# Kernel optimization log

Hardware: AMD Instinct MI355X
Metric: run time of the kernel (lower is better)

The kernel has to match this reference:

```python
import jax, jax.numpy as jnp
import numpy as np

N = 200_000   # num_nodes
E = 100_000   # events per direction
D = 128       # memory_dim
F = 128       # event feature dim
T = 128       # time encoding dim


def setup_inputs() -> dict:
    key = jax.random.key(0)
    ks = jax.random.split(key, 12)
    src = jax.random.randint(ks[0], (E,), 0, N)
    dst = jax.random.randint(ks[1], (E,), 0, N)
    t = jax.random.uniform(ks[2], (E,)) * 1000.0
    feat = jax.random.normal(ks[3], (E, F))
    memory = jax.random.normal(ks[4], (N, D)) * 0.1
    last_update = jnp.zeros((N,), dtype=jnp.float32)
    time_w = jax.random.normal(ks[5], (T,)) * 0.1
    time_b = jax.random.normal(ks[6], (T,)) * 0.1
    M = 2 * D + T + F  # message dim = 512
    w_ih = jax.random.normal(ks[7], (3 * D, M)) * 0.02
    w_hh = jax.random.normal(ks[8], (3 * D, D)) * 0.02
    b_ih = jnp.zeros((3 * D,), dtype=jnp.float32)
    b_hh = jnp.zeros((3 * D,), dtype=jnp.float32)
    return {
        "memory": memory, "last_update": last_update, "t": t, "feat": feat,
        "time_w": time_w, "time_b": time_b,
        "w_ih": w_ih, "w_hh": w_hh, "b_ih": b_ih, "b_hh": b_hh,
        "src": src, "dst": dst,
    }


def time_encode(dt, w, b):
    # TGN/TGAT-style cosine time encoding: [E] -> [E, T]
    return jnp.cos(dt[:, None] * w[None, :] + b[None, :])


def gru_cell(x, h, w_ih, w_hh, b_ih, b_hh):
    # Standard torch.nn.GRUCell math (gates ordered r, z, n).
    gi = x @ w_ih.T + b_ih  # [N, 3D]
    gh = h @ w_hh.T + b_hh  # [N, 3D]
    i_r, i_z, i_n = jnp.split(gi, 3, axis=-1)
    h_r, h_z, h_n = jnp.split(gh, 3, axis=-1)
    r = jax.nn.sigmoid(i_r + h_r)
    z = jax.nn.sigmoid(i_z + h_z)
    n = jnp.tanh(i_n + r * h_n)
    return (1.0 - z) * n + z * h


def reference(memory, last_update, t, feat, time_w, time_b,
              w_ih, w_hh, b_ih, b_hh, src, dst):
    # --- message functions (identity = concat), both directions ---
    s_msg = jnp.concatenate(
        [memory[src], memory[dst], time_encode(t - last_update[src], time_w, time_b), feat], axis=-1)
    d_msg = jnp.concatenate(
        [memory[dst], memory[src], time_encode(t - last_update[dst], time_w, time_b), feat], axis=-1)

    nodes = jnp.concatenate([src, dst], axis=0)        # [2E]
    te = jnp.concatenate([t, t], axis=0)               # [2E]
    msg = jnp.concatenate([s_msg, d_msg], axis=0)      # [2E, M]

    # --- 'last' aggregator: per-node argmax over event time (scatter_max) ---
    # Stable sort by time; segment_max over sorted positions yields, per node,
    # the latest event (ties broken toward the later original index).
    perm = jnp.argsort(te, stable=True)                # [2E]
    pos = jnp.arange(2 * E)
    best_pos = jax.ops.segment_max(pos, nodes[perm], num_segments=N)  # [N], intmin if empty
    has_msg = best_pos >= 0
    best = perm[jnp.clip(best_pos, 0)]                 # [N] event index of latest msg

    agg_msg = msg[best]                                # [N, M] gather
    max_t = te[best]                                   # [N]

    # --- GRU memory update + masked scatter back into memory ---
    new_mem = gru_cell(agg_msg, memory, w_ih, w_hh, b_ih, b_hh)
    new_memory = jnp.where(has_msg[:, None], new_mem, memory)
    new_last_update = jnp.where(has_msg, max_t, last_update)
    return new_memory, new_last_update
```

## Files before the change

### kernel.cpp

```cpp
#include <hip/hip_runtime.h>
#include <hip/hip_bf16.h>
#include <stdint.h>

typedef __hip_bfloat16 bf16;
typedef unsigned long long u64;
typedef unsigned int u32;
typedef short short8 __attribute__((ext_vector_type(8)));
typedef float f32x4 __attribute__((ext_vector_type(4)));

#define D_ 128
#define K_ 640
#define BM 64
#define BN 128
#define BK 64
#define BM2 32

__device__ __forceinline__ float bf2f(bf16 v) { return __bfloat162float(v); }
__device__ __forceinline__ u32 fbits(float f) { union { float f; u32 u; } c; c.f = f; return c.u; }
__device__ __forceinline__ u32 pk2(float a, float b) {
  union { bf16 h; unsigned short s; } x, y;
  x.h = __float2bfloat16(a); y.h = __float2bfloat16(b);
  return (u32)x.s | ((u32)y.s << 16);
}
template<bool F32>
__device__ __forceinline__ float ldE(const void* p, size_t i) {
  return F32 ? ((const float*)p)[i] : bf2f(((const bf16*)p)[i]);
}
template<bool F32>
__device__ __forceinline__ void stE(void* p, size_t i, float v) {
  if (F32) ((float*)p)[i] = v; else ((bf16*)p)[i] = __float2bfloat16(v);
}
template<bool F32>
__device__ __forceinline__ uint4 ld8(const void* base, size_t elemOff) {
  if (!F32) {
    return *(const uint4*)((const bf16*)base + elemOff);
  } else {
    const float4* p = (const float4*)((const float*)base + elemOff);
    float4 v0 = p[0], v1 = p[1];
    uint4 o; o.x = pk2(v0.x, v0.y); o.y = pk2(v0.z, v0.w);
    o.z = pk2(v1.x, v1.y); o.w = pk2(v1.z, v1.w);
    return o;
  }
}
template<bool F32>
__device__ __forceinline__ void stage8(const void* base, size_t elemOff, bf16* dst) {
  *(uint4*)dst = ld8<F32>(base, elemOff);
}
__device__ __forceinline__ void gl_lds16(const void* g, void* l) {
  __builtin_amdgcn_global_load_lds(
      (const __attribute__((address_space(1))) unsigned int*)g,
      (__attribute__((address_space(3))) unsigned int*)l, 16, 0, 0);
}

__global__ void k_prep(u64* __restrict__ key, u32* __restrict__ cnt, int N,
                       const u32* __restrict__ mem_w, const u32* __restrict__ t_w,
                       u32* __restrict__ flag) {
  int i = blockIdx.x * blockDim.x + threadIdx.x;
  if (i < N) key[i] = 0ull;
  if (i == 0) {
    *cnt = 0u;
    int ok = 1;
    for (int k = 0; k < 64; ++k) {
      u32 w = mem_w[k];
      if ((w & 0x7fffu) > 0x4300u) ok = 0;
      if (((w >> 16) & 0x7fffu) > 0x4300u) ok = 0;
    }
    for (int k = 0; k < 16; ++k) {
      u32 w = t_w[k];
      if ((w & 0xffffu) > 0x4480u) ok = 0;
      if ((w >> 16) > 0x4480u) ok = 0;
    }
    *flag = ok ? 0u : 1u;
  }
}

__global__ void k_scat(const int* __restrict__ src, const int* __restrict__ dst,
                       const void* __restrict__ t, const u32* __restrict__ flag,
                       u64* __restrict__ key, int E) {
  int i = blockIdx.x * blockDim.x + threadIdx.x;
  if (i >= 2 * E) return;
  int e = (i < E) ? i : i - E;
  int node = (i < E) ? src[e] : dst[e];
  float tv = (*flag) ? ((const float*)t)[e] : bf2f(((const bf16*)t)[e]);
  u64 k = ((u64)fbits(tv) << 32) | (u64)(u32)(i + 1);
  atomicMax(&key[node], k);
}

__global__ void k_pack(const void* __restrict__ wih, const void* __restrict__ whh,
                       const u32* __restrict__ flag, bf16* __restrict__ wpk) {
  int gid = blockIdx.x * 256 + threadIdx.x;
  if (gid >= 40960) return;
  int tile = gid >> 10, r = gid & 1023;
  int j = r >> 3, s = r & 7;
  int kc = tile >> 2, by = tile & 3;
  int kglob = kc * 64 + s * 8;
  int grp = j >> 5, gi = j & 31, gidx = 32 * by + gi;
  int srow = (grp == 0) ? gidx : (grp == 1) ? 128 + gidx : 256 + gidx;
  bool zero = (kglob < 512) ? (grp == 3) : (grp == 2);
  uint4 v;
  if (zero) v = (uint4){0u, 0u, 0u, 0u};
  else if (*flag) v = (kglob < 512) ? ld8<true>(wih, (size_t)srow * 512 + kglob)
                                    : ld8<true>(whh, (size_t)srow * 128 + (kglob - 512));
  else            v = (kglob < 512) ? ld8<false>(wih, (size_t)srow * 512 + kglob)
                                    : ld8<false>(whh, (size_t)srow * 128 + (kglob - 512));
  ((uint4*)wpk)[(size_t)tile * 1024 + ((j * 8 + s) ^ (j & 7))] = v;
}

template<bool F32>
__device__ __forceinline__ void compact_body(int n, const void* mem, const void* lastup,
                                             const void* t, const u64* key,
                                             int* list, u32* cnt, int use_list,
                                             void* out, int N, int E) {
  u32 b = (u32)key[n];
  if (b) {
    int pos = (int)(b - 1u);
    int e = (pos < E) ? pos : pos - E;
    stE<F32>(out, (size_t)N * D_ + n, ldE<F32>(t, e));
    if (use_list) { u32 idx = atomicAdd(cnt, 1u); list[idx] = n; }
  } else {
    if (F32) {
      const float4* s = (const float4*)((const float*)mem + (size_t)n * D_);
      float4* d = (float4*)((float*)out + (size_t)n * D_);
#pragma unroll
      for (int i = 0; i < 32; ++i) d[i] = s[i];
    } else {
      const uint4* s = (const uint4*)((const bf16*)mem + (size_t)n * D_);
      uint4* d = (uint4*)((bf16*)out + (size_t)n * D_);
#pragma unroll
      for (int i = 0; i < 16; ++i) d[i] = s[i];
    }
    stE<F32>(out, (size_t)N * D_ + n, ldE<F32>(lastup, n));
  }
}
__global__ void k_compact(const void* mem, const void* lastup, const void* t,
                          const u32* __restrict__ flag, const u64* __restrict__ key,
                          int* list, u32* cnt, int use_list,
                          void* out, int N, int E) {
  int n = blockIdx.x * blockDim.x + threadIdx.x;
  if (n >= N) return;
  if (*flag) compact_body<true>(n, mem, lastup, t, key, list, cnt, use_list, out, N, E);
  else       compact_body<false>(n, mem, lastup, t, key, list, cnt, use_list, out, N, E);
}

template<bool F32>
__device__ __forceinline__ uint4 a_fetch(int kc, int tid,
    const void* mem, const void* feat,
    const int* s_node, const int* s_e, const int* s_oth,
    const float* s_dt, const float* s_tw, const float* s_tb) {
  int r = tid >> 3, s = tid & 7;
  int k0 = kc * 64 + s * 8;
  if (k0 < 128) return ld8<F32>(mem, (size_t)s_node[r] * D_ + k0);
  if (k0 < 256) return ld8<F32>(mem, (size_t)s_oth[r] * D_ + (k0 - 128));
  if (k0 < 384) {
    float dtv = s_dt[r];
    float f[8];
#pragma unroll
    for (int q = 0; q < 8; ++q) {
      int j = k0 - 256 + q;
      f[q] = cosf(fmaf(dtv, s_tw[j], s_tb[j]));
    }
    uint4 o; o.x = pk2(f[0], f[1]); o.y = pk2(f[2], f[3]);
    o.z = pk2(f[4], f[5]); o.w = pk2(f[6], f[7]);
    return o;
  }
  if (k0 < 512) return ld8<F32>(feat, (size_t)s_e[r] * D_ + (k0 - 384));
  return ld8<F32>(mem, (size_t)s_node[r] * D_ + (k0 - 512));
}

__device__ __forceinline__ void b_issue(const bf16* __restrict__ wpk, int tile,
                                        bf16* BsBuf, int tid) {
  int w = tid >> 6;
  const bf16* g = wpk + (size_t)tile * 8192 + w * 2048 + (tid & 63) * 8;
  bf16* l = BsBuf + w * 2048;
#pragma unroll
  for (int i = 0; i < 4; ++i)
    gl_lds16(g + i * 512, l + i * 512);
}

template<bool F32>
__device__ __forceinline__ void gemm2_body(
    const void* mem, const void* lastup, const void* t, const void* feat,
    const int* __restrict__ src, const int* __restrict__ dst,
    const bf16* __restrict__ wpk,
    const void* bih, const void* bhh, const void* tw, const void* tb,
    const u64* __restrict__ key, const int* __restrict__ list,
    const u32* __restrict__ cnt, int use_list,
    void* out, int N, int E,
    char* smem, int* s_node, int* s_e, int* s_oth, int* s_act,
    float* s_dt, float* s_tw, float* s_tb) {
  const int tid = threadIdx.x;
  const int bx = blockIdx.x;
  bf16 (*As)[BM2][72] = (bf16 (*)[BM2][72])smem;
  bf16* BsBase = (bf16*)(smem + 9216);
  float (*Gs)[133] = (float (*)[133])smem;

  b_issue(wpk, 0, BsBase, tid);

  if (tid < BM2) {
    int r = tid, row = BM2 * bx + r, node = -1;
    if (use_list) { int c = (int)*cnt; if (row < c) node = list[row]; }
    else if (row < N) node = row;
    int act = 0, e = 0, oth = 0; float dtv = 0.f;
    if (node >= 0) {
      u32 b = (u32)key[node];
      if (b) {
        act = 1;
        int pos = (int)(b - 1u);
        if (pos < E) { e = pos; oth = dst[e]; } else { e = pos - E; oth = src[e]; }
        dtv = ldE<F32>(t, e) - ldE<F32>(lastup, node);
      }
    }
    if (node < 0) node = 0;
    s_node[r] = node; s_e[r] = e; s_oth[r] = oth; s_act[r] = act; s_dt[r] = dtv;
  }
  if (tid < 128) s_tw[tid] = ldE<F32>(tw, tid);
  else           s_tb[tid - 128] = ldE<F32>(tb, tid - 128);
  __syncthreads();

  {
    uint4 a0 = a_fetch<F32>(0, tid, mem, feat, s_node, s_e, s_oth, s_dt, s_tw, s_tb);
    *(uint4*)&As[0][tid >> 3][(tid & 7) * 8] = a0;
  }
  __syncthreads();

  const int w = tid >> 6, l = tid & 63;
  const int mrow = l & 15, quad = l >> 4;
  f32x4 acc[4][2][2];
#pragma unroll
  for (int by = 0; by < 4; ++by)
#pragma unroll
    for (int mi = 0; mi < 2; ++mi)
#pragma unroll
      for (int ni = 0; ni < 2; ++ni) acc[by][mi][ni] = (f32x4){0.f, 0.f, 0.f, 0.f};

  uint4 apre = (uint4){0u, 0u, 0u, 0u};
#pragma unroll 1
  for (int kc = 0; kc < K_ / 64; ++kc) {
    const int ka = kc & 1;
    short8 a[2][2];
#pragma unroll
    for (int by = 0; by < 4; ++by) {
      const int tile = kc * 4 + by;
      if (by == 0) {
        if (kc + 1 < 10)
          apre = a_fetch<F32>(kc + 1, tid, mem, feat, s_node, s_e, s_oth, s_dt, s_tw, s_tb);
      }
      if (tile + 1 < 40)
        b_issue(wpk, tile + 1, BsBase + (((by & 1) ^ 1) << 13), tid);
      if (by == 0) {
#pragma unroll
        for (int ks2 = 0; ks2 < 2; ++ks2)
#pragma unroll
          for (int mi = 0; mi < 2; ++mi)
            a[ks2][mi] = *(const short8*)((const char*)&As[ka][0][0] +
                             (16 * mi + mrow) * 144 + ks2 * 64 + quad * 16);
      }
      const char* Bsb = (const char*)(BsBase + ((by & 1) << 13));
      short8 b[2][2];
#pragma unroll
      for (int ks2 = 0; ks2 < 2; ++ks2)
#pragma unroll
        for (int ni = 0; ni < 2; ++ni) {
          int j = 32 * w + 16 * ni + mrow;
          int off = (j * 128 + ks2 * 64 + quad * 16) ^ ((j & 7) << 4);
          b[ks2][ni] = *(const short8*)(Bsb + off);
        }
#pragma unroll
      for (int ks2 = 0; ks2 < 2; ++ks2)
#pragma unroll
        for (int mi = 0; mi < 2; ++mi)
#pragma unroll
          for (int ni = 0; ni < 2; ++ni)
            acc[by][mi][ni] = __builtin_amdgcn_mfma_f32_16x16x32_bf16(
                a[ks2][mi], b[ks2][ni], acc[by][mi][ni], 0, 0, 0);
      if (by == 3 && kc + 1 < 10)
        *(uint4*)&As[ka ^ 1][tid >> 3][(tid & 7) * 8] = apre;
      __syncthreads();
    }
  }

#pragma unroll
  for (int by = 0; by < 4; ++by) {
#pragma unroll
    for (int mi = 0; mi < 2; ++mi)
#pragma unroll
      for (int ni = 0; ni < 2; ++ni)
#pragma unroll
        for (int reg = 0; reg < 4; ++reg)
          Gs[16 * mi + quad * 4 + reg][32 * w + 16 * ni + mrow] = acc[by][mi][ni][reg];
    __syncthreads();
    {
      int r = tid >> 3, giB = (tid & 7) * 4;
      if (s_act[r]) {
        int node = s_node[r];
#pragma unroll
        for (int q = 0; q < 4; ++q) {
          int gi = giB + q, gidx = 32 * by + gi;
          float rp  = Gs[r][gi]      + ldE<F32>(bih, gidx)       + ldE<F32>(bhh, gidx);
          float zp  = Gs[r][32 + gi] + ldE<F32>(bih, 128 + gidx) + ldE<F32>(bhh, 128 + gidx);
          float inp = Gs[r][64 + gi] + ldE<F32>(bih, 256 + gidx);
          float hnp = Gs[r][96 + gi] + ldE<F32>(bhh, 256 + gidx);
          float rg = 1.f / (1.f + expf(-rp));
          float zg = 1.f / (1.f + expf(-zp));
          float ng = tanhf(inp + rg * hnp);
          float h = ldE<F32>(mem, (size_t)node * D_ + gidx);
          stE<F32>(out, (size_t)node * D_ + gidx, (1.f - zg) * ng + zg * h);
        }
      }
    }
    __syncthreads();
  }
}

__global__ __launch_bounds__(256, 3)
void k_gemm2(const void* mem, const void* lastup, const void* t, const void* feat,
             const int* src, const int* dst, const bf16* wpk,
             const void* bih, const void* bhh, const void* tw, const void* tb,
             const u32* __restrict__ flag, const u64* __restrict__ key,
             const int* __restrict__ list, const u32* __restrict__ cnt, int use_list,
             void* out, int N, int E) {
  if (use_list && (int)*cnt <= BM2 * (int)blockIdx.x) return;
  __shared__ __align__(16) char smem[41984];
  __shared__ int s_node[BM2], s_e[BM2], s_oth[BM2], s_act[BM2];
  __shared__ float s_dt[BM2], s_tw[128], s_tb[128];
  if (*flag)
    gemm2_body<true>(mem, lastup, t, feat, src, dst, wpk, bih, bhh, tw, tb,
                     key, list, cnt, use_list, out, N, E,
                     smem, s_node, s_e, s_oth, s_act, s_dt, s_tw, s_tb);
  else
    gemm2_body<false>(mem, lastup, t, feat, src, dst, wpk, bih, bhh, tw, tb,
                      key, list, cnt, use_list, out, N, E,
                      smem, s_node, s_e, s_oth, s_act, s_dt, s_tw, s_tb);
}

template<bool F32>
__device__ __forceinline__ void gemm_body(
    const void* mem, const void* lastup, const void* t, const void* feat,
    const int* __restrict__ src, const int* __restrict__ dst,
    const void* wih, const void* whh, const void* bih, const void* bhh,
    const void* tw, const void* tb,
    const u64* __restrict__ key, const int* __restrict__ list,
    const u32* __restrict__ cnt, int use_list,
    void* out, int N, int E,
    bf16 (*As)[72], bf16 (*Bs)[72], float (*Gs)[132],
    int* s_node, int* s_e, int* s_oth, int* s_act, float* s_dt) {
  const int tid = threadIdx.x;
  const int bx = blockIdx.x, by = blockIdx.y;

  if (tid < BM) {
    int r = tid;
    int row = BM * bx + r;
    int node = -1;
    if (use_list) { int c = (int)*cnt; if (row < c) node = list[row]; }
    else if (row < N) node = row;
    int act = 0, e = 0, oth = 0; float dtv = 0.f;
    if (node >= 0) {
      u32 b = (u32)key[node];
      if (b) {
        act = 1;
        int pos = (int)(b - 1u);
        if (pos < E) { e = pos; oth = dst[e]; } else { e = pos - E; oth = src[e]; }
        dtv = ldE<F32>(t, e) - ldE<F32>(lastup, node);
      }
    }
    if (node < 0) node = 0;
    s_node[r] = node; s_e[r] = e; s_oth[r] = oth; s_act[r] = act; s_dt[r] = dtv;
  }

  const int w = tid >> 6, l = tid & 63;
  const int mrow = l & 15, quad = l >> 4;
  f32x4 acc[4][2];
#pragma unroll
  for (int mi = 0; mi < 4; ++mi)
#pragma unroll
    for (int ni = 0; ni < 2; ++ni) acc[mi][ni] = (f32x4){0.f, 0.f, 0.f, 0.f};

#pragma unroll 1
  for (int kc = 0; kc < K_ / BK; ++kc) {
    __syncthreads();
#pragma unroll
    for (int it = 0; it < 2; ++it) {
      int task = tid + 256 * it;
      int r = task >> 3, s = task & 7;
      int k0 = kc * BK + s * 8;
      bf16* dstp = &As[r][s * 8];
      if (k0 < 128)       stage8<F32>(mem,  (size_t)s_node[r] * D_ + k0, dstp);
      else if (k0 < 256)  stage8<F32>(mem,  (size_t)s_oth[r] * D_ + (k0 - 128), dstp);
      else if (k0 < 384) {
        float dtv = s_dt[r];
        float f[8];
#pragma unroll
        for (int q = 0; q < 8; ++q) {
          int j = k0 - 256 + q;
          f[q] = cosf(fmaf(dtv, ldE<F32>(tw, j), ldE<F32>(tb, j)));
        }
        uint4 o; o.x = pk2(f[0], f[1]); o.y = pk2(f[2], f[3]);
        o.z = pk2(f[4], f[5]); o.w = pk2(f[6], f[7]);
        *(uint4*)dstp = o;
      }
      else if (k0 < 512)  stage8<F32>(feat, (size_t)s_e[r] * D_ + (k0 - 384), dstp);
      else                stage8<F32>(mem,  (size_t)s_node[r] * D_ + (k0 - 512), dstp);
    }
#pragma unroll
    for (int it = 0; it < 4; ++it) {
      int task = tid + 256 * it;
      int j = task >> 3, s = task & 7;
      int k0 = kc * BK + s * 8;
      int grp = j >> 5, gi = j & 31;
      int gidx = 32 * by + gi;
      bf16* dstp = &Bs[j][s * 8];
      if (k0 < 512) {
        if (grp == 3) { *(uint4*)dstp = (uint4){0, 0, 0, 0}; }
        else {
          int srow = (grp == 0) ? gidx : (grp == 1) ? 128 + gidx : 256 + gidx;
          stage8<F32>(wih, (size_t)srow * 512 + k0, dstp);
        }
      } else {
        if (grp == 2) { *(uint4*)dstp = (uint4){0, 0, 0, 0}; }
        else {
          int srow = (grp == 0) ? gidx : (grp == 1) ? 128 + gidx : 256 + gidx;
          stage8<F32>(whh, (size_t)srow * D_ + (k0 - 512), dstp);
        }
      }
    }
    __syncthreads();
#pragma unroll
    for (int ks = 0; ks < BK; ks += 32) {
      short8 a[4], b[2];
#pragma unroll
      for (int mi = 0; mi < 4; ++mi)
        a[mi] = *(const short8*)&As[16 * mi + mrow][ks + quad * 8];
#pragma unroll
      for (int ni = 0; ni < 2; ++ni)
        b[ni] = *(const short8*)&Bs[32 * w + 16 * ni + mrow][ks + quad * 8];
#pragma unroll
      for (int mi = 0; mi < 4; ++mi)
#pragma unroll
        for (int ni = 0; ni < 2; ++ni)
          acc[mi][ni] = __builtin_amdgcn_mfma_f32_16x16x32_bf16(a[mi], b[ni], acc[mi][ni], 0, 0, 0);
    }
  }

#pragma unroll
  for (int mi = 0; mi < 4; ++mi)
#pragma unroll
    for (int ni = 0; ni < 2; ++ni)
#pragma unroll
      for (int reg = 0; reg < 4; ++reg)
        Gs[16 * mi + quad * 4 + reg][32 * w + 16 * ni + mrow] = acc[mi][ni][reg];
  __syncthreads();

  {
    int r = tid >> 2;
    int giB = (tid & 3) * 8;
    if (s_act[r]) {
      int node = s_node[r];
#pragma unroll
      for (int q = 0; q < 8; ++q) {
        int gi = giB + q;
        int gidx = 32 * by + gi;
        float rp  = Gs[r][gi]       + ldE<F32>(bih, gidx)       + ldE<F32>(bhh, gidx);
        float zp  = Gs[r][32 + gi]  + ldE<F32>(bih, 128 + gidx) + ldE<F32>(bhh, 128 + gidx);
        float inp = Gs[r][64 + gi]  + ldE<F32>(bih, 256 + gidx);
        float hnp = Gs[r][96 + gi]  + ldE<F32>(bhh, 256 + gidx);
        float rg = 1.f / (1.f + expf(-rp));
        float zg = 1.f / (1.f + expf(-zp));
        float ng = tanhf(inp + rg * hnp);
        float h = ldE<F32>(mem, (size_t)node * D_ + gidx);
        stE<F32>(out, (size_t)node * D_ + gidx, (1.f - zg) * ng + zg * h);
      }
    }
  }
}

__global__ __launch_bounds__(256)
void k_gemm_fb(const void* mem, const void* lastup, const void* t, const void* feat,
               const int* src, const int* dst,
               const void* wih, const void* whh, const void* bih, const void* bhh,
               const void* tw, const void* tb,
               const u32* __restrict__ flag, const u64* __restrict__ key,
               const int* __restrict__ list, const u32* __restrict__ cnt, int use_list,
               void* out, int N, int E) {
  if (use_list && (int)*cnt <= BM * (int)blockIdx.x) return;

  __shared__ __align__(16) bf16 As[BM][72];
  __shared__ __align__(16) bf16 Bs[BN][72];
  __shared__ __align__(16) float Gs[BM][132];
  __shared__ int s_node[BM], s_e[BM], s_oth[BM], s_act[BM];
  __shared__ float s_dt[BM];

  if (*flag)
    gemm_body<true>(mem, lastup, t, feat, src, dst, wih, whh, bih, bhh, tw, tb,
                    key, list, cnt, use_list, out, N, E,
                    As, Bs, Gs, s_node, s_e, s_oth, s_act, s_dt);
  else
    gemm_body<false>(mem, lastup, t, feat, src, dst, wih, whh, bih, bhh, tw, tb,
                     key, list, cnt, use_list, out, N, E,
                     As, Bs, Gs, s_node, s_e, s_oth, s_act, s_dt);
}

extern "C" void kernel_launch(void* const* d_in, const int* in_sizes, int n_in,
                              void* d_out, int out_size, void* d_ws, size_t ws_size,
                              hipStream_t stream) {
  const void* mem    = d_in[0];
  const void* lastup = d_in[1];
  const void* t      = d_in[2];
  const void* feat   = d_in[3];
  const void* tw     = d_in[4];
  const void* tb     = d_in[5];
  const void* wih    = d_in[6];
  const void* whh    = d_in[7];
  const void* bih    = d_in[8];
  const void* bhh    = d_in[9];
  const int*  src    = (const int*)d_in[10];
  const int*  dst    = (const int*)d_in[11];

  int N = in_sizes[0] / D_;
  int E = in_sizes[2];

  char* ws = (char*)d_ws;
  size_t off = 0;
  u32* flag = (u32*)(ws + off); off += 16;
  u32* cnt  = (u32*)(ws + off); off += 16;
  u64* key  = (u64*)(ws + off); off += (size_t)N * 8;
  int* list = (int*)(ws + off); off += (size_t)N * 4;
  int use_list = (ws_size >= off) ? 1 : 0;
  bf16* wpk = (bf16*)(ws + off); off += (size_t)512 * 640 * 2;
  int use_wpk = (ws_size >= off) ? 1 : 0;

  const int thr = 256;
  int nb  = (N + thr - 1) / thr;
  int eb  = (2 * E + thr - 1) / thr;

  k_prep<<<dim3(nb), dim3(thr), 0, stream>>>(key, cnt, N, (const u32*)mem, (const u32*)t, flag);
  k_scat<<<dim3(eb), dim3(thr), 0, stream>>>(src, dst, t, flag, key, E);
  if (use_wpk)
    k_pack<<<dim3(160), dim3(thr), 0, stream>>>(wih, whh, flag, wpk);
  k_compact<<<dim3(nb), dim3(thr), 0, stream>>>(mem, lastup, t, flag, key,
                                                list, cnt, use_list, d_out, N, E);
  if (use_wpk) {
    int mt = (N + BM2 - 1) / BM2;
    k_gemm2<<<dim3(mt), dim3(thr), 0, stream>>>(
        mem, lastup, t, feat, src, dst, wpk, bih, bhh, tw, tb,
        flag, key, list, cnt, use_list, d_out, N, E);
  } else {
    int mt = (N + BM - 1) / BM;
    k_gemm_fb<<<dim3(mt, 4), dim3(thr), 0, stream>>>(
        mem, lastup, t, feat, src, dst, wih, whh, bih, bhh, tw, tb,
        flag, key, list, cnt, use_list, d_out, N, E);
  }
}
```

Before: 516.8 us.

## Fold hidden-state GEMM into input weights to shrink K from 640 to 512

The memory row appears in both the message (src memory at k<128) and the hidden state, so w_hh's r/z columns are pre-added into w_ih's first 128 columns in the packed weights. The n-gate hidden part is placed in a fourth column group that only uses k<128, which lets wave 3 skip MFMAs and B loads after the first two K chunks. This cuts the K loop from 10 to 8 chunks and drops the redundant memory reload. It also replaces per-node atomicAdd list compaction with a wave-ballot prefix plus one atomic per block, and raises MFMA issue priority. Summing the weights in bf16 changes rounding slightly.

```diff
diff --git a/kernel.cpp b/kernel.cpp
--- a/kernel.cpp
+++ b/kernel.cpp
@@ -9,10 +9,10 @@
 typedef float f32x4 __attribute__((ext_vector_type(4)));
 
 #define D_ 128
-#define K_ 640
 #define BM 64
 #define BN 128
 #define BK 64
+#define KFB 640
 #define BM2 32
 
 __device__ __forceinline__ float bf2f(bf16 v) { return __bfloat162float(v); }
@@ -86,37 +86,68 @@
   atomicMax(&key[node], k);
 }
 
-__global__ void k_pack(const void* __restrict__ wih, const void* __restrict__ whh,
-                       const u32* __restrict__ flag, bf16* __restrict__ wpk) {
+__global__ void k_pack2(const void* __restrict__ wih, const void* __restrict__ whh,
+                        const u32* __restrict__ flag, bf16* __restrict__ wpk) {
   int gid = blockIdx.x * 256 + threadIdx.x;
-  if (gid >= 40960) return;
+  if (gid >= 32768) return;
   int tile = gid >> 10, r = gid & 1023;
   int j = r >> 3, s = r & 7;
   int kc = tile >> 2, by = tile & 3;
   int kglob = kc * 64 + s * 8;
   int grp = j >> 5, gi = j & 31, gidx = 32 * by + gi;
-  int srow = (grp == 0) ? gidx : (grp == 1) ? 128 + gidx : 256 + gidx;
-  bool zero = (kglob < 512) ? (grp == 3) : (grp == 2);
-  uint4 v;
-  if (zero) v = (uint4){0u, 0u, 0u, 0u};
-  else if (*flag) v = (kglob < 512) ? ld8<true>(wih, (size_t)srow * 512 + kglob)
-                                    : ld8<true>(whh, (size_t)srow * 128 + (kglob - 512));
-  else            v = (kglob < 512) ? ld8<false>(wih, (size_t)srow * 512 + kglob)
-                                    : ld8<false>(whh, (size_t)srow * 128 + (kglob - 512));
-  ((uint4*)wpk)[(size_t)tile * 1024 + ((j * 8 + s) ^ (j & 7))] = v;
-}
-
-template<bool F32>
-__device__ __forceinline__ void compact_body(int n, const void* mem, const void* lastup,
+  bool F = (*flag != 0);
+  float f[8];
+#pragma unroll
+  for (int q = 0; q < 8; ++q) {
+    int k = kglob + q;
+    float v = 0.f;
+    if (grp < 3) {
+      int srow = grp * 128 + gidx;
+      v = F ? ldE<true>(wih, (size_t)srow * 512 + k) : ldE<false>(wih, (size_t)srow * 512 + k);
+      if (k < 128 && grp < 2)
+        v += F ? ldE<true>(whh, (size_t)srow * 128 + k) : ldE<false>(whh, (size_t)srow * 128 + k);
+    } else if (k < 128) {
+      v = F ? ldE<true>(whh, (size_t)(256 + gidx) * 128 + k)
+            : ldE<false>(whh, (size_t)(256 + gidx) * 128 + k);
+    }
+    f[q] = v;
+  }
+  uint4 o; o.x = pk2(f[0], f[1]); o.y = pk2(f[2], f[3]);
+  o.z = pk2(f[4], f[5]); o.w = pk2(f[6], f[7]);
+  ((uint4*)wpk)[(size_t)tile * 1024 + ((j * 8 + s) ^ (j & 7))] = o;
+}
+
+template<bool F32>
+__device__ __forceinline__ void compact_body(int n, bool nvalid,
+                                             const void* mem, const void* lastup,
                                              const void* t, const u64* key,
                                              int* list, u32* cnt, int use_list,
-                                             void* out, int N, int E) {
-  u32 b = (u32)key[n];
-  if (b) {
+                                             void* out, int N, int E, u32* s_wb) {
+  u32 b = 0;
+  if (nvalid) b = (u32)key[n];
+  bool active = nvalid && (b != 0u);
+  if (use_list) {
+    u64 mask = __ballot(active);
+    int lane = threadIdx.x & 63, w = threadIdx.x >> 6;
+    if (lane == 0) s_wb[w] = (u32)__popcll(mask);
+    __syncthreads();
+    if (threadIdx.x == 0) {
+      u32 tot = s_wb[0] + s_wb[1] + s_wb[2] + s_wb[3];
+      u32 base = tot ? atomicAdd(cnt, tot) : 0u;
+      u32 acc0 = base;
+      for (int i = 0; i < 4; ++i) { u32 c = s_wb[i]; s_wb[i] = acc0; acc0 += c; }
+    }
+    __syncthreads();
+    if (active) {
+      u32 idx = s_wb[w] + (u32)__popcll(mask & ((1ull << lane) - 1ull));
+      list[idx] = n;
+    }
+  }
+  if (!nvalid) return;
+  if (active) {
     int pos = (int)(b - 1u);
     int e = (pos < E) ? pos : pos - E;
     stE<F32>(out, (size_t)N * D_ + n, ldE<F32>(t, e));
-    if (use_list) { u32 idx = atomicAdd(cnt, 1u); list[idx] = n; }
   } else {
     if (F32) {
       const float4* s = (const float4*)((const float*)mem + (size_t)n * D_);
@@ -136,19 +167,20 @@
                           const u32* __restrict__ flag, const u64* __restrict__ key,
                           int* list, u32* cnt, int use_list,
                           void* out, int N, int E) {
+  __shared__ u32 s_wb[4];
   int n = blockIdx.x * blockDim.x + threadIdx.x;
-  if (n >= N) return;
-  if (*flag) compact_body<true>(n, mem, lastup, t, key, list, cnt, use_list, out, N, E);
-  else       compact_body<false>(n, mem, lastup, t, key, list, cnt, use_list, out, N, E);
-}
-
-template<bool F32>
-__device__ __forceinline__ uint4 a_fetch(int kc, int tid,
+  bool nvalid = (n < N);
+  if (*flag) compact_body<true>(n, nvalid, mem, lastup, t, key, list, cnt, use_list, out, N, E, s_wb);
+  else       compact_body<false>(n, nvalid, mem, lastup, t, key, list, cnt, use_list, out, N, E, s_wb);
+}
+
+template<bool F32>
+__device__ __forceinline__ uint4 a_fetch(int kcn, int tid,
     const void* mem, const void* feat,
     const int* s_node, const int* s_e, const int* s_oth,
     const float* s_dt, const float* s_tw, const float* s_tb) {
   int r = tid >> 3, s = tid & 7;
-  int k0 = kc * 64 + s * 8;
+  int k0 = kcn * 64 + s * 8;
   if (k0 < 128) return ld8<F32>(mem, (size_t)s_node[r] * D_ + k0);
   if (k0 < 256) return ld8<F32>(mem, (size_t)s_oth[r] * D_ + (k0 - 128));
   if (k0 < 384) {
@@ -163,8 +195,7 @@
     o.z = pk2(f[4], f[5]); o.w = pk2(f[6], f[7]);
     return o;
   }
-  if (k0 < 512) return ld8<F32>(feat, (size_t)s_e[r] * D_ + (k0 - 384));
-  return ld8<F32>(mem, (size_t)s_node[r] * D_ + (k0 - 512));
+  return ld8<F32>(feat, (size_t)s_e[r] * D_ + (k0 - 384));
 }
 
 __device__ __forceinline__ void b_issue(const bf16* __restrict__ wpk, int tile,
@@ -225,6 +256,7 @@
 
   const int w = tid >> 6, l = tid & 63;
   const int mrow = l & 15, quad = l >> 4;
+  const bool w3 = (w == 3);
   f32x4 acc[4][2][2];
 #pragma unroll
   for (int by = 0; by < 4; ++by)
@@ -235,17 +267,17 @@
 
   uint4 apre = (uint4){0u, 0u, 0u, 0u};
 #pragma unroll 1
-  for (int kc = 0; kc < K_ / 64; ++kc) {
+  for (int kc = 0; kc < 8; ++kc) {
     const int ka = kc & 1;
     short8 a[2][2];
 #pragma unroll
     for (int by = 0; by < 4; ++by) {
       const int tile = kc * 4 + by;
       if (by == 0) {
-        if (kc + 1 < 10)
+        if (kc + 1 < 8)
           apre = a_fetch<F32>(kc + 1, tid, mem, feat, s_node, s_e, s_oth, s_dt, s_tw, s_tb);
       }
-      if (tile + 1 < 40)
+      if (tile + 1 < 32 && !(w3 && (tile + 1) >= 8))
         b_issue(wpk, tile + 1, BsBase + (((by & 1) ^ 1) << 13), tid);
       if (by == 0) {
 #pragma unroll
@@ -255,25 +287,29 @@
             a[ks2][mi] = *(const short8*)((const char*)&As[ka][0][0] +
                              (16 * mi + mrow) * 144 + ks2 * 64 + quad * 16);
       }
-      const char* Bsb = (const char*)(BsBase + ((by & 1) << 13));
-      short8 b[2][2];
-#pragma unroll
-      for (int ks2 = 0; ks2 < 2; ++ks2)
-#pragma unroll
-        for (int ni = 0; ni < 2; ++ni) {
-          int j = 32 * w + 16 * ni + mrow;
-          int off = (j * 128 + ks2 * 64 + quad * 16) ^ ((j & 7) << 4);
-          b[ks2][ni] = *(const short8*)(Bsb + off);
-        }
-#pragma unroll
-      for (int ks2 = 0; ks2 < 2; ++ks2)
-#pragma unroll
-        for (int mi = 0; mi < 2; ++mi)
-#pragma unroll
-          for (int ni = 0; ni < 2; ++ni)
-            acc[by][mi][ni] = __builtin_amdgcn_mfma_f32_16x16x32_bf16(
-                a[ks2][mi], b[ks2][ni], acc[by][mi][ni], 0, 0, 0);
-      if (by == 3 && kc + 1 < 10)
+      if (!(w3 && kc >= 2)) {
+        const char* Bsb = (const char*)(BsBase + ((by & 1) << 13));
+        short8 b[2][2];
+#pragma unroll
+        for (int ks2 = 0; ks2 < 2; ++ks2)
+#pragma unroll
+          for (int ni = 0; ni < 2; ++ni) {
+            int j = 32 * w + 16 * ni + mrow;
+            int off = (j * 128 + ks2 * 64 + quad * 16) ^ ((j & 7) << 4);
+            b[ks2][ni] = *(const short8*)(Bsb + off);
+          }
+        __builtin_amdgcn_s_setprio(1);
+#pragma unroll
+        for (int ks2 = 0; ks2 < 2; ++ks2)
+#pragma unroll
+          for (int mi = 0; mi < 2; ++mi)
+#pragma unroll
+            for (int ni = 0; ni < 2; ++ni)
+              acc[by][mi][ni] = __builtin_amdgcn_mfma_f32_16x16x32_bf16(
+                  a[ks2][mi], b[ks2][ni], acc[by][mi][ni], 0, 0, 0);
+        __builtin_amdgcn_s_setprio(0);
+      }
+      if (by == 3 && kc + 1 < 8)
         *(uint4*)&As[ka ^ 1][tid >> 3][(tid & 7) * 8] = apre;
       __syncthreads();
     }
@@ -376,7 +412,7 @@
     for (int ni = 0; ni < 2; ++ni) acc[mi][ni] = (f32x4){0.f, 0.f, 0.f, 0.f};
 
 #pragma unroll 1
-  for (int kc = 0; kc < K_ / BK; ++kc) {
+  for (int kc = 0; kc < KFB / BK; ++kc) {
     __syncthreads();
 #pragma unroll
     for (int it = 0; it < 2; ++it) {
@@ -525,20 +561,20 @@
   u64* key  = (u64*)(ws + off); off += (size_t)N * 8;
   int* list = (int*)(ws + off); off += (size_t)N * 4;
   int use_list = (ws_size >= off) ? 1 : 0;
-  bf16* wpk = (bf16*)(ws + off); off += (size_t)512 * 640 * 2;
-  int use_wpk = (ws_size >= off) ? 1 : 0;
+  bf16* wpk = (bf16*)(ws + off); off += (size_t)32 * 8192 * 2;
+  int use2 = (ws_size >= off) ? 1 : 0;
 
   const int thr = 256;
-  int nb  = (N + thr - 1) / thr;
-  int eb  = (2 * E + thr - 1) / thr;
+  int nb = (N + thr - 1) / thr;
+  int eb = (2 * E + thr - 1) / thr;
 
   k_prep<<<dim3(nb), dim3(thr), 0, stream>>>(key, cnt, N, (const u32*)mem, (const u32*)t, flag);
   k_scat<<<dim3(eb), dim3(thr), 0, stream>>>(src, dst, t, flag, key, E);
-  if (use_wpk)
-    k_pack<<<dim3(160), dim3(thr), 0, stream>>>(wih, whh, flag, wpk);
+  if (use2)
+    k_pack2<<<dim3(128), dim3(thr), 0, stream>>>(wih, whh, flag, wpk);
   k_compact<<<dim3(nb), dim3(thr), 0, stream>>>(mem, lastup, t, flag, key,
                                                 list, cnt, use_list, d_out, N, E);
-  if (use_wpk) {
+  if (use2) {
     int mt = (N + BM2 - 1) / BM2;
     k_gemm2<<<dim3(mt), dim3(thr), 0, stream>>>(
         mem, lastup, t, feat, src, dst, wpk, bih, bhh, tw, tb,
```

Measured after the change: 480.2 us. 7.1% less time.
